# Kernel tuning notes

Hardware: AMD Instinct MI355X
Metric: run time of the kernel (lower is better)

Reference implementation:

```python
import jax, jax.numpy as jnp
import numpy as np

N, E, F_IN, H, NC, NG = 50000, 800000, 256, 64, 4, 64

def setup_inputs() -> dict:
    key = jax.random.key(0)
    ks = jax.random.split(key, 12)
    inp = {
        'x': jax.random.normal(ks[0], (N, F_IN), dtype=jnp.float32),
        'edge_index': jax.random.randint(ks[1], (2, E), 0, N, dtype=jnp.int64),
        'batch': jnp.sort(jax.random.randint(ks[2], (N,), 0, NG, dtype=jnp.int64)),
        # GCNConv layer 1 and 2 (weight [in,out] + bias), Glorot-ish scale
        'W1': jax.random.normal(ks[3], (F_IN, H), dtype=jnp.float32) / np.sqrt(F_IN),
        'b1': jnp.zeros((H,), dtype=jnp.float32),
        'W2': jax.random.normal(ks[4], (H, H), dtype=jnp.float32) / np.sqrt(H),
        'b2': jnp.zeros((H,), dtype=jnp.float32),
        # MLP head
        'fc1_w': jax.random.normal(ks[5], (H, 128), dtype=jnp.float32) / np.sqrt(H),
        'fc1_b': jnp.zeros((128,), dtype=jnp.float32),
        'fc2_w': jax.random.normal(ks[6], (128, NC), dtype=jnp.float32) / np.sqrt(128),
        'fc2_b': jnp.zeros((NC,), dtype=jnp.float32),
    }
    return inp

def _gcn_conv(x, src, dst, W, b, n_nodes):
    # PyG GCNConv: add self-loops, symmetric norm D^-1/2 (A+I) D^-1/2, then X W + b
    h = x @ W  # [N, out]
    deg = jax.ops.segment_sum(jnp.ones_like(dst, dtype=h.dtype), dst, num_segments=n_nodes)
    dinv = jnp.where(deg > 0, jax.lax.rsqrt(deg), 0.0)
    norm = dinv[src] * dinv[dst]  # [E+N]
    msg = h[src] * norm[:, None]
    out = jax.ops.segment_sum(msg, dst, num_segments=n_nodes)
    return out + b

def reference(x, edge_index, batch, W1, b1, W2, b2, fc1_w, fc1_b, fc2_w, fc2_b):
    n = x.shape[0]
    loops = jnp.arange(n, dtype=edge_index.dtype)
    src = jnp.concatenate([edge_index[0], loops])
    dst = jnp.concatenate([edge_index[1], loops])
    h = jax.nn.relu(_gcn_conv(x, src, dst, W1, b1, n))
    h = jax.nn.relu(_gcn_conv(h, src, dst, W2, b2, n))
    # global_mean_pool over graph ids
    sums = jax.ops.segment_sum(h, batch, num_segments=NG)
    cnts = jax.ops.segment_sum(jnp.ones((n,), h.dtype), batch, num_segments=NG)
    pooled = sums / jnp.maximum(cnts, 1.0)[:, None]  # [NG, H]
    z = jax.nn.relu(pooled @ fc1_w + fc1_b)
    # dropout in eval mode = identity
    return z @ fc2_w + fc2_b  # [NG, NC]
```

## Files before the change

kernel.cpp:

```cpp
#include <hip/hip_runtime.h>


#define TPB 256
#define CHUNK_A 4096
#define BCAP 4608

typedef unsigned short bfu;
typedef __attribute__((ext_vector_type(8))) short s16x8;
typedef __attribute__((ext_vector_type(4))) float f32x4;

__device__ __forceinline__ float bf2f(bfu u) {
    union { unsigned u32; float f; } c; c.u32 = ((unsigned)u) << 16; return c.f;
}
__device__ __forceinline__ bfu f2bf(float f) {
    union { float f; unsigned u; } c; c.f = f;
    unsigned r = 0x7FFFu + ((c.u >> 16) & 1u);
    return (bfu)((c.u + r) >> 16);
}
__device__ __forceinline__ float blo(unsigned w) {
    union { unsigned u32; float f; } c; c.u32 = w << 16; return c.f;
}
__device__ __forceinline__ float bhi(unsigned w) {
    union { unsigned u32; float f; } c; c.u32 = w & 0xFFFF0000u; return c.f;
}
__device__ __forceinline__ void split_bf(float x, bfu& h, bfu& l) {
    h = f2bf(x);
    l = f2bf(x - bf2f(h));
}


__global__ __launch_bounds__(TPB) void k_passA(const int* __restrict__ srcv,
                                               const int* __restrict__ dstv, int E,
                                               int* __restrict__ gcur,
                                               int* __restrict__ staged, int nbuck) {
    __shared__ int pk[CHUNK_A];
    __shared__ int hist[256];
    __shared__ int ebase[256];
    __shared__ int gbase[256];
    __shared__ int lcur[256];
    int t = threadIdx.x;
    int e0 = blockIdx.x * CHUNK_A;
    int e1 = e0 + CHUNK_A; if (e1 > E) e1 = E;

    hist[t] = 0; lcur[t] = 0;
    __syncthreads();
    for (int i = e0 + t; i < e1; i += TPB) atomicAdd(&hist[dstv[i] >> 8], 1);
    __syncthreads();
    int v = hist[t];
    ebase[t] = v;
    __syncthreads();
    for (int off = 1; off < 256; off <<= 1) {
        int u = (t >= off) ? ebase[t - off] : 0;
        __syncthreads();
        ebase[t] += u;
        __syncthreads();
    }
    ebase[t] -= v;
    if (t < nbuck && v > 0) gbase[t] = t * BCAP + atomicAdd(&gcur[t], v);
    __syncthreads();
    for (int i = e0 + t; i < e1; i += TPB) {
        int d = dstv[i];
        int s = srcv[i];
        int b = d >> 8;
        int r = atomicAdd(&lcur[b], 1);
        pk[ebase[b] + r] = (s << 8) | (d & 255);
    }
    __syncthreads();
    int wave = t >> 6, lane = t & 63;
    for (int b = wave; b < nbuck; b += 4) {
        int c = hist[b];
        int lb = ebase[b];
        int gb = gbase[b];
        for (int j = lane; j < c; j += 64) staged[gb + j] = pk[lb + j];
    }
}


__global__ __launch_bounds__(TPB) void k_passB(const int* __restrict__ staged,
                                               const int* __restrict__ gcur,
                                               int* __restrict__ csr_off,
                                               int* __restrict__ csr_src,
                                               float* __restrict__ dinv,
                                               int n, int nbuck) {
    __shared__ int pk[BCAP];
    __shared__ int soff[256];
    __shared__ int hist[256];
    __shared__ int nbase[256];
    __shared__ int cur[256];
    int b = blockIdx.x;
    int n0 = b << 8;
    int n1 = n0 + 256; if (n1 > n) n1 = n;
    int cnt = gcur[b];
    int t = threadIdx.x;

    int cv = (t < nbuck) ? gcur[t] : 0;
    soff[t] = cv;
    hist[t] = 0; cur[t] = 0;
    __syncthreads();
    for (int off = 1; off < 256; off <<= 1) {
        int u = (t >= off) ? soff[t - off] : 0;
        __syncthreads();
        soff[t] += u;
        __syncthreads();
    }
    int base = soff[b] - cnt;

    for (int i = t; i < cnt; i += TPB) pk[i] = staged[b * BCAP + i];
    __syncthreads();
    for (int i = t; i < cnt; i += TPB) atomicAdd(&hist[pk[i] & 255], 1);
    __syncthreads();
    int v = hist[t];
    nbase[t] = v;
    __syncthreads();
    for (int off = 1; off < 256; off <<= 1) {
        int u = (t >= off) ? nbase[t - off] : 0;
        __syncthreads();
        nbase[t] += u;
        __syncthreads();
    }
    nbase[t] -= v;
    if (n0 + t < n1) {
        csr_off[n0 + t] = base + nbase[t];
        dinv[n0 + t] = rsqrtf((float)(v + 1));
    }
    if (b == nbuck - 1 && t == 0) csr_off[n] = base + cnt;
    __syncthreads();
    for (int i = t; i < cnt; i += TPB) {
        int p = pk[i];
        int dloc = p & 255;
        int r = atomicAdd(&cur[dloc], 1);
        csr_src[base + nbase[dloc] + r] = p >> 8;
    }
}


__device__ __forceinline__ int swz(int rc, int k) {
    return rc * 64 + (k ^ ((rc & 7) << 3));
}

template <int K, bool BF16A>
__global__ __launch_bounds__(TPB) void k_gemm(const void* __restrict__ Av,
                                              const float* __restrict__ W,
                                              const float* __restrict__ dinv,
                                              bfu* __restrict__ C, int n) {
    __shared__ __align__(16) ushort Ah[128 * 64];
    __shared__ __align__(16) ushort Al[BF16A ? 64 : 128 * 64];
    __shared__ __align__(16) ushort Bh[64 * 64];
    __shared__ __align__(16) ushort Bl[64 * 64];

    const int t = threadIdx.x;
    const int wave = t >> 6, lane = t & 63;
    const int rbase = blockIdx.x * 128;

    f32x4 acc[2][4];
#pragma unroll
    for (int i = 0; i < 2; i++)
#pragma unroll
        for (int j = 0; j < 4; j++) acc[i][j] = {0.f, 0.f, 0.f, 0.f};

    for (int kc = 0; kc < K; kc += 64) {
        {
            int c = t & 63;
            int kg = (t >> 6) << 4;
#pragma unroll
            for (int q = 0; q < 4; q++) {
                ushort4 h4, l4;
#pragma unroll
                for (int j = 0; j < 4; j++) {
                    float w = W[(size_t)(kc + kg + q * 4 + j) * 64 + c];
                    bfu hh, ll; split_bf(w, hh, ll);
                    ((bfu*)&h4)[j] = hh;
                    ((bfu*)&l4)[j] = ll;
                }
                *(ushort4*)&Bh[swz(c, kg + q * 4)] = h4;
                *(ushort4*)&Bl[swz(c, kg + q * 4)] = l4;
            }
        }
        if (!BF16A) {
            const float* A = (const float*)Av;
#pragma unroll
            for (int q = 0; q < 8; q++) {
                int idx = q * 256 + t;
                int row = idx >> 4;
                int k4 = (idx & 15) << 2;
                int r = rbase + row;
                float4 xv = make_float4(0.f, 0.f, 0.f, 0.f);
                if (r < n) xv = *(const float4*)&A[(size_t)r * K + kc + k4];
                ushort4 h4, l4;
                split_bf(xv.x, ((bfu*)&h4)[0], ((bfu*)&l4)[0]);
                split_bf(xv.y, ((bfu*)&h4)[1], ((bfu*)&l4)[1]);
                split_bf(xv.z, ((bfu*)&h4)[2], ((bfu*)&l4)[2]);
                split_bf(xv.w, ((bfu*)&h4)[3], ((bfu*)&l4)[3]);
                *(ushort4*)&Ah[swz(row, k4)] = h4;
                *(ushort4*)&Al[swz(row, k4)] = l4;
            }
        } else {
            const bfu* A = (const bfu*)Av;
#pragma unroll
            for (int q = 0; q < 4; q++) {
                int idx = q * 256 + t;
                int row = idx >> 3;
                int k8 = (idx & 7) << 3;
                int r = rbase + row;
                uint4 v = make_uint4(0u, 0u, 0u, 0u);
                if (r < n) v = *(const uint4*)(A + (size_t)r * 64 + k8);
                *(uint2*)&Ah[swz(row, k8)]     = make_uint2(v.x, v.y);
                *(uint2*)&Ah[swz(row, k8 + 4)] = make_uint2(v.z, v.w);
            }
        }
        __syncthreads();

        const int rl = lane & 15;
        const int kg8 = (lane >> 4) << 3;
#pragma unroll
        for (int ks = 0; ks < 2; ks++) {
            int k0 = ks * 32 + kg8;
            s16x8 a_h[2], a_l[2], b_h[4], b_l[4];
#pragma unroll
            for (int rt = 0; rt < 2; rt++) {
                int row = wave * 32 + rt * 16 + rl;
                a_h[rt] = *(const s16x8*)&Ah[swz(row, k0)];
                if (!BF16A) a_l[rt] = *(const s16x8*)&Al[swz(row, k0)];
            }
#pragma unroll
            for (int ct = 0; ct < 4; ct++) {
                int cc = ct * 16 + rl;
                b_h[ct] = *(const s16x8*)&Bh[swz(cc, k0)];
                b_l[ct] = *(const s16x8*)&Bl[swz(cc, k0)];
            }
#pragma unroll
            for (int rt = 0; rt < 2; rt++)
#pragma unroll
                for (int ct = 0; ct < 4; ct++) {
                    acc[rt][ct] = __builtin_amdgcn_mfma_f32_16x16x32_bf16(
                        a_h[rt], b_h[ct], acc[rt][ct], 0, 0, 0);
                    acc[rt][ct] = __builtin_amdgcn_mfma_f32_16x16x32_bf16(
                        a_h[rt], b_l[ct], acc[rt][ct], 0, 0, 0);
                    if (!BF16A)
                        acc[rt][ct] = __builtin_amdgcn_mfma_f32_16x16x32_bf16(
                            a_l[rt], b_h[ct], acc[rt][ct], 0, 0, 0);
                }
        }
        __syncthreads();
    }

    const int rl = lane & 15;
    const int rq = (lane >> 4) << 2;
#pragma unroll
    for (int rt = 0; rt < 2; rt++) {
#pragma unroll
        for (int reg = 0; reg < 4; reg++) {
            int r = rbase + wave * 32 + rt * 16 + rq + reg;
            if (r < n) {
                float d = dinv[r];
#pragma unroll
                for (int ct = 0; ct < 4; ct++) {
                    C[(size_t)r * 64 + ct * 16 + rl] = f2bf(acc[rt][ct][reg] * d);
                }
            }
        }
    }
}


#define AGG_ISSUE8(G) \
    { \
        _Pragma("unroll") \
        for (int i = 0; i < 8; i++) { \
            int e = 2 * ((G) * 8 + i) + half; \
            int s = __shfl(myidx, e); \
            gb[(G) * 8 + i] = *(const unsigned*)(hs + (size_t)((e < rem) ? s : node) * 64 + fl); \
        } \
    }

#define AGG_ADD8(G) \
    { \
        _Pragma("unroll") \
        for (int i = 0; i < 8; i++) { \
            int e = 2 * ((G) * 8 + i) + half; \
            unsigned g = gb[(G) * 8 + i]; \
            ax += (e < rem) ? blo(g) : 0.f; \
            ay += (e < rem) ? bhi(g) : 0.f; \
        } \
    }

template <bool FUSE>
__global__ __launch_bounds__(TPB) void k_agg(const bfu* __restrict__ hs,
                                             const int* __restrict__ csr_off,
                                             const int* __restrict__ csr_src,
                                             const float* __restrict__ dinv,
                                             const float* __restrict__ bias,
                                             const float* __restrict__ W2,
                                             bfu* __restrict__ out, int n) {
    __shared__ float rowbuf[4][64];
    int wv = threadIdx.x >> 6;
    int node = blockIdx.x * 4 + wv;
    int lane = threadIdx.x & 63;
    int half = lane >> 5;
    int fl = (lane & 31) * 2;
    if (node >= n) return;
    int p0 = csr_off[node];
    int p1 = csr_off[node + 1];
    int deg = p1 - p0;
    float d = dinv[node];

    unsigned gself = *(const unsigned*)(hs + (size_t)node * 64 + fl);

    float ax = 0.f, ay = 0.f;
    for (int base = 0; base < deg; base += 32) {
        int rem = deg - base;
        int li = p0 + base + (lane & 31);
        int myidx = (li < p1) ? csr_src[li] : node;
        unsigned gb[16];
        AGG_ISSUE8(0)
        if (rem > 16) AGG_ISSUE8(1)
        AGG_ADD8(0)
        if (rem > 16) AGG_ADD8(1)
    }
    if (half == 0) { ax += blo(gself); ay += bhi(gself); }

    ax += __shfl_xor(ax, 32);
    ay += __shfl_xor(ay, 32);

    float vx = fmaxf(d * ax + bias[fl + 0], 0.f);
    float vy = fmaxf(d * ay + bias[fl + 1], 0.f);
    if (!FUSE) {
        if (half == 0) {
            ushort2 o;
            o.x = f2bf(vx);
            o.y = f2bf(vy);
            *(ushort2*)(out + (size_t)node * 64 + fl) = o;
        }
    } else {
        if (half == 0) { rowbuf[wv][fl] = vx; rowbuf[wv][fl + 1] = vy; }
        __builtin_amdgcn_wave_barrier();
        float a = 0.f;
#pragma unroll 16
        for (int k = 0; k < 64; k++) a += rowbuf[wv][k] * W2[k * 64 + lane];
        out[(size_t)node * 64 + lane] = f2bf(d * a);
    }
}


__global__ __launch_bounds__(TPB) void k_pool(const bfu* __restrict__ h,
                                              const int* __restrict__ batch, int n,
                                              float* __restrict__ gsum,
                                              int* __restrict__ gcnt) {
    const int CH = 16;
    int wid = blockIdx.x * 4 + (threadIdx.x >> 6);
    int lane = threadIdx.x & 63;
    int i0 = wid * CH;
    if (i0 >= n) return;
    int i1 = i0 + CH; if (i1 > n) i1 = n;
    int g0 = batch[i0];
    int g1 = batch[i1 - 1];
    if (g0 == g1) {
        float acc = 0.f;
#pragma unroll
        for (int i = 0; i < CH; i++) {
            int idx = i0 + i;
            if (idx < i1) acc += bf2f(h[(size_t)idx * 64 + lane]);
        }
        atomicAdd(&gsum[g0 * 64 + lane], acc);
        if (lane == 0) atomicAdd(&gcnt[g0], i1 - i0);
    } else {
        int cur = g0;
        float acc = 0.f;
        int cnt = 0;
        for (int i = i0; i < i1; i++) {
            int g = batch[i];
            if (g != cur) {
                atomicAdd(&gsum[cur * 64 + lane], acc);
                if (lane == 0) atomicAdd(&gcnt[cur], cnt);
                acc = 0.f; cnt = 0; cur = g;
            }
            acc += bf2f(h[(size_t)i * 64 + lane]);
            cnt++;
        }
        atomicAdd(&gsum[cur * 64 + lane], acc);
        if (lane == 0) atomicAdd(&gcnt[cur], cnt);
    }
}


__global__ __launch_bounds__(TPB) void k_head1(const float* __restrict__ gsum,
                                               const int* __restrict__ gcnt,
                                               const float* __restrict__ fc1w,
                                               const float* __restrict__ fc1b,
                                               float* __restrict__ z) {
    int t = threadIdx.x;
    int g = blockIdx.x * 2 + (t >> 7);
    int o = t & 127;
    int c = gcnt[g]; if (c < 1) c = 1;
    float inv = 1.0f / (float)c;
    float a = fc1b[o];
#pragma unroll 16
    for (int j = 0; j < 64; j++) {
        float pj = gsum[g * 64 + j] * inv;
        a += pj * fc1w[j * 128 + o];
    }
    z[g * 128 + o] = fmaxf(a, 0.f);
}


__global__ __launch_bounds__(TPB) void k_head2(const float* __restrict__ z,
                                               const float* __restrict__ fc2w,
                                               const float* __restrict__ fc2b,
                                               float* __restrict__ out) {
    int t = threadIdx.x;
    int g = t >> 2, c = t & 3;
    float a = fc2b[c];
#pragma unroll 16
    for (int o = 0; o < 128; o++) a += z[g * 128 + o] * fc2w[o * 4 + c];
    out[t] = a;
}


extern "C" void kernel_launch(void* const* d_in, const int* in_sizes, int n_in,
                              void* d_out, int out_size, void* d_ws, size_t ws_size,
                              hipStream_t stream) {
    const float* x    = (const float*)d_in[0];
    const int*   ei   = (const int*)d_in[1];
    const int*   batch= (const int*)d_in[2];
    const float* W1   = (const float*)d_in[3];
    const float* b1   = (const float*)d_in[4];
    const float* W2   = (const float*)d_in[5];
    const float* b2   = (const float*)d_in[6];
    const float* fc1w = (const float*)d_in[7];
    const float* fc1b = (const float*)d_in[8];
    const float* fc2w = (const float*)d_in[9];
    const float* fc2b = (const float*)d_in[10];

    const int n = in_sizes[2];
    const int E = in_sizes[1] / 2;
    const int* srcv = ei;
    const int* dstv = ei + E;
    const int nbuck = (n + 255) >> 8;

    char* w = (char*)d_ws;
    int*   gcur   = (int*)w;            w += 256 * 4;
    int*   gcnt   = (int*)w;            w += 64 * 4;
    float* gsum   = (float*)w;          w += 64 * 64 * 4;
    size_t zbytes = (size_t)w - (size_t)d_ws;
    int*   csr_off= (int*)w;            w += (size_t)(n + 1) * 4;
    float* dinv   = (float*)w;          w += (size_t)n * 4;
    int*   csr_src= (int*)w;            w += (size_t)E * 4;
    int*   staged = (int*)w;            w += (size_t)nbuck * BCAP * 4;
    float* zbuf   = (float*)w;          w += 64 * 128 * 4;
    w = (char*)(((size_t)w + 255) & ~(size_t)255);
    bfu* hs = (bfu*)w;                  w += (size_t)n * 64 * 2;
    w = (char*)(((size_t)w + 255) & ~(size_t)255);
    bfu* hb = (bfu*)w;                  w += (size_t)n * 64 * 2;

    hipMemsetAsync(d_ws, 0, zbytes, stream);

    int gA = (E + CHUNK_A - 1) / CHUNK_A;
    k_passA<<<gA, TPB, 0, stream>>>(srcv, dstv, E, gcur, staged, nbuck);
    k_passB<<<nbuck, TPB, 0, stream>>>(staged, gcur, csr_off, csr_src, dinv, n, nbuck);

    int gRows = (n + 127) / 128;
    int gNode = (n + 3) / 4;
    k_gemm<256, false><<<gRows, TPB, 0, stream>>>(x, W1, dinv, hs, n);
    k_agg<true><<<gNode, TPB, 0, stream>>>(hs, csr_off, csr_src, dinv, b1, W2, hb, n);
    k_agg<false><<<gNode, TPB, 0, stream>>>(hb, csr_off, csr_src, dinv, b2, nullptr, hs, n);

    int nwaves16 = (n + 15) / 16;
    k_pool<<<(nwaves16 + 3) / 4, TPB, 0, stream>>>(hs, batch, n, gsum, gcnt);
    k_head1<<<32, TPB, 0, stream>>>(gsum, gcnt, fc1w, fc1b, zbuf);
    k_head2<<<1, TPB, 0, stream>>>(zbuf, fc2w, fc2b, (float*)d_out);
}
```

Baseline: 261.8 us.

## Remap aggregation lanes to 16-byte row loads across eight neighbors

```diff
diff --git a/kernel.cpp b/kernel.cpp
--- a/kernel.cpp
+++ b/kernel.cpp
@@ -263,26 +263,12 @@
 }
 
 
-#define AGG_ISSUE8(G) \
-    { \
-        _Pragma("unroll") \
-        for (int i = 0; i < 8; i++) { \
-            int e = 2 * ((G) * 8 + i) + half; \
-            int s = __shfl(myidx, e); \
-            gb[(G) * 8 + i] = *(const unsigned*)(hs + (size_t)((e < rem) ? s : node) * 64 + fl); \
-        } \
-    }
-
-#define AGG_ADD8(G) \
-    { \
-        _Pragma("unroll") \
-        for (int i = 0; i < 8; i++) { \
-            int e = 2 * ((G) * 8 + i) + half; \
-            unsigned g = gb[(G) * 8 + i]; \
-            ax += (e < rem) ? blo(g) : 0.f; \
-            ay += (e < rem) ? bhi(g) : 0.f; \
-        } \
-    }
+__device__ __forceinline__ void acc_u4(float* acc, uint4 q) {
+    acc[0] += blo(q.x); acc[1] += bhi(q.x);
+    acc[2] += blo(q.y); acc[3] += bhi(q.y);
+    acc[4] += blo(q.z); acc[5] += bhi(q.z);
+    acc[6] += blo(q.w); acc[7] += bhi(q.w);
+}
 
 template <bool FUSE>
 __global__ __launch_bounds__(TPB) void k_agg(const bfu* __restrict__ hs,
@@ -296,43 +282,76 @@
     int wv = threadIdx.x >> 6;
     int node = blockIdx.x * 4 + wv;
     int lane = threadIdx.x & 63;
-    int half = lane >> 5;
-    int fl = (lane & 31) * 2;
+    int g = lane >> 3;
+    int c = lane & 7;
     if (node >= n) return;
     int p0 = csr_off[node];
     int p1 = csr_off[node + 1];
     int deg = p1 - p0;
     float d = dinv[node];
 
-    unsigned gself = *(const unsigned*)(hs + (size_t)node * 64 + fl);
-
-    float ax = 0.f, ay = 0.f;
-    for (int base = 0; base < deg; base += 32) {
+    uint4 selfv = *(const uint4*)(hs + (size_t)node * 64 + c * 8);
+
+    float acc[8];
+#pragma unroll
+    for (int j = 0; j < 8; j++) acc[j] = 0.f;
+
+    for (int base = 0; base < deg; base += 16) {
         int rem = deg - base;
-        int li = p0 + base + (lane & 31);
-        int myidx = (li < p1) ? csr_src[li] : node;
-        unsigned gb[16];
-        AGG_ISSUE8(0)
-        if (rem > 16) AGG_ISSUE8(1)
-        AGG_ADD8(0)
-        if (rem > 16) AGG_ADD8(1)
-    }
-    if (half == 0) { ax += blo(gself); ay += bhi(gself); }
-
-    ax += __shfl_xor(ax, 32);
-    ay += __shfl_xor(ay, 32);
-
-    float vx = fmaxf(d * ax + bias[fl + 0], 0.f);
-    float vy = fmaxf(d * ay + bias[fl + 1], 0.f);
+        int li0 = p0 + base + g;
+        if (rem > 8) {
+            int li1 = li0 + 8;
+            int idx0 = csr_src[li0];
+            int idx1 = csr_src[li1 < p1 ? li1 : p0];
+            bool v1 = (8 + g) < rem;
+            uint4 q0 = *(const uint4*)(hs + (size_t)idx0 * 64 + c * 8);
+            uint4 q1 = *(const uint4*)(hs + (size_t)(v1 ? idx1 : node) * 64 + c * 8);
+            if (!v1) q1 = make_uint4(0u, 0u, 0u, 0u);
+            acc_u4(acc, q0);
+            acc_u4(acc, q1);
+        } else {
+            bool v0 = g < rem;
+            int idx0 = csr_src[li0 < p1 ? li0 : p0];
+            uint4 q0 = *(const uint4*)(hs + (size_t)(v0 ? idx0 : node) * 64 + c * 8);
+            if (!v0) q0 = make_uint4(0u, 0u, 0u, 0u);
+            acc_u4(acc, q0);
+        }
+    }
+
+#pragma unroll
+    for (int j = 0; j < 8; j++) {
+        acc[j] += __shfl_xor(acc[j], 8);
+        acc[j] += __shfl_xor(acc[j], 16);
+        acc[j] += __shfl_xor(acc[j], 32);
+    }
+    acc_u4(acc, selfv);
+
+    float4 b0 = *(const float4*)&bias[c * 8];
+    float4 b1 = *(const float4*)&bias[c * 8 + 4];
+    float v[8];
+    v[0] = fmaxf(d * acc[0] + b0.x, 0.f);
+    v[1] = fmaxf(d * acc[1] + b0.y, 0.f);
+    v[2] = fmaxf(d * acc[2] + b0.z, 0.f);
+    v[3] = fmaxf(d * acc[3] + b0.w, 0.f);
+    v[4] = fmaxf(d * acc[4] + b1.x, 0.f);
+    v[5] = fmaxf(d * acc[5] + b1.y, 0.f);
+    v[6] = fmaxf(d * acc[6] + b1.z, 0.f);
+    v[7] = fmaxf(d * acc[7] + b1.w, 0.f);
+
     if (!FUSE) {
-        if (half == 0) {
-            ushort2 o;
-            o.x = f2bf(vx);
-            o.y = f2bf(vy);
-            *(ushort2*)(out + (size_t)node * 64 + fl) = o;
+        if (g == 0) {
+            uint4 o;
+            o.x = (unsigned)f2bf(v[0]) | ((unsigned)f2bf(v[1]) << 16);
+            o.y = (unsigned)f2bf(v[2]) | ((unsigned)f2bf(v[3]) << 16);
+            o.z = (unsigned)f2bf(v[4]) | ((unsigned)f2bf(v[5]) << 16);
+            o.w = (unsigned)f2bf(v[6]) | ((unsigned)f2bf(v[7]) << 16);
+            *(uint4*)(out + (size_t)node * 64 + c * 8) = o;
         }
     } else {
-        if (half == 0) { rowbuf[wv][fl] = vx; rowbuf[wv][fl + 1] = vy; }
+        if (g == 0) {
+            *(float4*)&rowbuf[wv][c * 8]     = make_float4(v[0], v[1], v[2], v[3]);
+            *(float4*)&rowbuf[wv][c * 8 + 4] = make_float4(v[4], v[5], v[6], v[7]);
+        }
         __builtin_amdgcn_wave_barrier();
         float a = 0.f;
 #pragma unroll 16
```

Measured after the change: 252.4 us. -3.6%, faster.
